# Kernel optimization log

Hardware: AMD Instinct MI355X
Metric: run time of the kernel (lower is better)

Reference implementation:

```python
import jax, jax.numpy as jnp
import numpy as np

B, S, HID = 2, 2048, 2048
H, D = 16, 128
BASE = 10000.0
NEG = -1e9


def _rope_tables(seq_len, dim, dtype):
    inv_freq = 1.0 / (BASE ** (jnp.arange(0, dim, 2, dtype=jnp.float32) / dim))
    pos = jnp.arange(seq_len, dtype=jnp.float32)
    freqs = jnp.einsum('s,d->sd', pos, inv_freq)          # [S, D/2]
    emb = jnp.concatenate([freqs, freqs], axis=-1)        # [S, D]
    return jnp.cos(emb).astype(dtype), jnp.sin(emb).astype(dtype)


def _rotate_half(x):
    x1, x2 = jnp.split(x, 2, axis=-1)
    return jnp.concatenate([-x2, x1], axis=-1)


def setup_inputs() -> dict:
    key = jax.random.key(0)
    k1, k2, k3 = jax.random.split(key, 3)
    x = jax.random.normal(k1, (B, S, HID), dtype=jnp.float32)
    w_qkv = jax.random.normal(k2, (HID, 3 * HID), dtype=jnp.float32) * (HID ** -0.5)
    w_out = jax.random.normal(k3, (HID, HID), dtype=jnp.float32) * (HID ** -0.5)
    return {"x": x, "w_qkv": w_qkv, "w_out": w_out}


def reference(x, w_qkv, w_out):
    b, s, _ = x.shape
    qkv = x @ w_qkv                                        # [B, S, 3*HID]
    qkv = qkv.reshape(b, s, 3, H, D).transpose(2, 0, 3, 1, 4)  # [3, B, H, S, D]
    q, k, v = qkv[0], qkv[1], qkv[2]
    cos, sin = _rope_tables(s, D, x.dtype)                 # [S, D]
    cos = cos[None, None]
    sin = sin[None, None]
    q = q * cos + _rotate_half(q) * sin
    k = k * cos + _rotate_half(k) * sin
    scale = 1.0 / np.sqrt(D)
    scores = jnp.einsum('bhqd,bhkd->bhqk', q, k) * scale   # [B, H, S, S]
    causal = jnp.triu(jnp.ones((s, s), dtype=bool), k=1)
    scores = jnp.where(causal[None, None], NEG, scores)
    attn = jax.nn.softmax(scores, axis=-1)
    out = jnp.einsum('bhqk,bhkd->bhqd', attn, v)           # [B, H, S, D]
    out = out.transpose(0, 2, 1, 3).reshape(b, s, H * D)
    return out @ w_out
```

## Files before the change

### kernel.cpp

```cpp
#include <hip/hip_runtime.h>
#include <hip/hip_bf16.h>

#define S_LEN 2048
#define HID_DIM 2048
#define NH 16
#define HD 128
#define N3 6144

typedef __bf16 bf16x8 __attribute__((ext_vector_type(8)));
typedef float f32x4 __attribute__((ext_vector_type(4)));
typedef float f32x16 __attribute__((ext_vector_type(16)));

#define MFMA16(a, b, c) __builtin_amdgcn_mfma_f32_16x16x32_bf16(a, b, c, 0, 0, 0)
#define MFMA32(a, b, c) __builtin_amdgcn_mfma_f32_32x32x16_bf16(a, b, c, 0, 0, 0)

__device__ __forceinline__ unsigned short f2bf(float f) {
  union { float f; unsigned u; } v; v.f = f;
  return (unsigned short)((v.u + 0x7fffu + ((v.u >> 16) & 1u)) >> 16);
}
__device__ __forceinline__ float bf2f(unsigned short h) {
  union { unsigned u; float f; } v; v.u = ((unsigned)h) << 16; return v.f;
}
__device__ __forceinline__ unsigned packbf2(float lo, float hi) {
  union { __hip_bfloat162 h2; unsigned u; } cv;
  cv.h2 = __float22bfloat162_rn(make_float2(lo, hi));
  return cv.u;
}
__device__ __forceinline__ void store_c(float* p, float v) { *p = v; }
__device__ __forceinline__ void store_c(unsigned short* p, float v) { *p = f2bf(v); }

__device__ __forceinline__ void async16(const void* g, void* l) {
  __builtin_amdgcn_global_load_lds((const __attribute__((address_space(1))) unsigned int*)g,
                                   (__attribute__((address_space(3))) unsigned int*)l,
                                   16, 0, 0);
}

template <int N> __device__ __forceinline__ void vmcnt();
template <> __device__ __forceinline__ void vmcnt<0>() { asm volatile("s_waitcnt vmcnt(0)" ::: "memory"); }
template <> __device__ __forceinline__ void vmcnt<5>() { asm volatile("s_waitcnt vmcnt(5)" ::: "memory"); }
template <> __device__ __forceinline__ void vmcnt<6>() { asm volatile("s_waitcnt vmcnt(6)" ::: "memory"); }

__global__ __launch_bounds__(256) void cast_bf16(const float4* __restrict__ src,
                                                 ushort4* __restrict__ dst) {
  int i = blockIdx.x * 256 + threadIdx.x;
  float4 v = src[i];
  ushort4 o;
  o.x = f2bf(v.x); o.y = f2bf(v.y); o.z = f2bf(v.z); o.w = f2bf(v.w);
  dst[i] = o;
}

__global__ __launch_bounds__(256) void transpose_cast(const float* __restrict__ src,
                                                      unsigned short* __restrict__ dst,
                                                      int R, int Ccols) {
  __shared__ float t[32][33];
  int ct = Ccols >> 5;
  int bx = blockIdx.x % ct, by = blockIdx.x / ct;
  int c0 = bx << 5, r0 = by << 5;
  int lx = threadIdx.x & 31, ly = threadIdx.x >> 5;
#pragma unroll
  for (int i = 0; i < 32; i += 8)
    t[ly + i][lx] = src[(long long)(r0 + ly + i) * Ccols + c0 + lx];
  __syncthreads();
#pragma unroll
  for (int i = 0; i < 32; i += 8)
    dst[(long long)(c0 + ly + i) * R + r0 + lx] = f2bf(t[lx][ly + i]);
}

__global__ __launch_bounds__(256) void rope_tables(float* __restrict__ cosT,
                                                   float* __restrict__ sinT) {
  int idx = blockIdx.x * 256 + threadIdx.x;
  int s = idx >> 6, i = idx & 63;
  float invf = powf(10000.0f, -(float)i * (1.0f / 64.0f));
  float a = (float)s * invf;
  cosT[idx] = cosf(a);
  sinT[idx] = sinf(a);
}

template <int BM, int BN, typename OutT>
__global__ __launch_bounds__(512) void gemm_pipe8(const unsigned short* __restrict__ A,
                                                  const unsigned short* __restrict__ Bt,
                                                  OutT* __restrict__ C,
                                                  int Mdim, int Ndim, int Kdim) {
  constexpr int WTM = BM / 2, WTN = BN / 4;
  constexpr int MREP = WTM / 16, NREP = WTN / 16;
  constexpr int AEL = BM * 64, BEL = BN * 64, BUFE = AEL + BEL;
  constexpr int AINST = BM / 64, BINST = BN / 64;
  constexpr int AHALF = BM / 128, BHALF = BN / 128;
  constexpr int VN = BN / 64 + BM / 128;
  __shared__ unsigned short smem[2 * BUFE];

  const int ntn = Ndim / BN;
  const int nwg = (Mdim / BM) * ntn;
  int bid = blockIdx.x;
  bid = (bid & 7) * (nwg >> 3) + (bid >> 3);
  const int tm = (bid / ntn) * BM;
  const int tn = (bid % ntn) * BN;

  const int tid = threadIdx.x;
  const int w = tid >> 6, l = tid & 63;
  const int g = l >> 4, cc = l & 15;
  const int wm = w >> 2, wn = w & 3;

  const int srow = tid >> 3;
  const int schunk = (tid & 7) ^ (srow & 7);
  const unsigned short* gA = A + (long long)(tm + srow) * Kdim + schunk * 8;
  const unsigned short* gB = Bt + (long long)(tn + srow) * Kdim + schunk * 8;

  const int ch0 = ((g) ^ (cc & 7)) << 3;
  const int ch1 = ((4 + g) ^ (cc & 7)) << 3;

  f32x4 acc[MREP][NREP] = {};
  bf16x8 a[MREP / 2][2], b[NREP][2];

  const int nk = Kdim >> 6;

#define STAGE_A(kt2, s) \
  async16(gA + (long long)(s) * 64 * Kdim + ((long long)(kt2) << 6), \
          smem + ((kt2) & 1) * BUFE + (s) * 4096 + w * 512)
#define STAGE_B(kt2, s) \
  async16(gB + (long long)(s) * 64 * Kdim + ((long long)(kt2) << 6), \
          smem + ((kt2) & 1) * BUFE + AEL + (s) * 4096 + w * 512)

#pragma unroll
  for (int s = 0; s < AINST; ++s) STAGE_A(0, s);
#pragma unroll
  for (int s = 0; s < BINST; ++s) STAGE_B(0, s);
#pragma unroll
  for (int s = 0; s < BINST; ++s) STAGE_B(1, s);
#pragma unroll
  for (int s = 0; s < AHALF; ++s) STAGE_A(1, s);
  vmcnt<VN>();
  __builtin_amdgcn_s_barrier();

  for (int kt = 0; kt < nk; ++kt) {
    const int buf = kt & 1;
    const unsigned short* Ab = smem + buf * BUFE + (wm * WTM) * 64;
    const unsigned short* Bb = smem + buf * BUFE + AEL + (wn * WTN) * 64;

#pragma unroll
    for (int i = 0; i < MREP / 2; ++i) {
      const int r = (i * 16 + cc) << 6;
      a[i][0] = *(const bf16x8*)(Ab + r + ch0);
      a[i][1] = *(const bf16x8*)(Ab + r + ch1);
    }
#pragma unroll
    for (int j = 0; j < NREP; ++j) {
      const int r = (j * 16 + cc) << 6;
      b[j][0] = *(const bf16x8*)(Bb + r + ch0);
      b[j][1] = *(const bf16x8*)(Bb + r + ch1);
    }
    if (kt + 1 < nk) {
#pragma unroll
      for (int s = AHALF; s < AINST; ++s) STAGE_A(kt + 1, s);
    }
    __builtin_amdgcn_s_barrier();
    __builtin_amdgcn_s_setprio(1);
#pragma unroll
    for (int i = 0; i < MREP / 2; ++i)
#pragma unroll
      for (int j = 0; j < NREP / 2; ++j) {
        acc[i][j] = MFMA16(a[i][0], b[j][0], acc[i][j]);
        acc[i][j] = MFMA16(a[i][1], b[j][1], acc[i][j]);
      }
    __builtin_amdgcn_s_setprio(0);
    __builtin_amdgcn_s_barrier();

    if (kt + 2 < nk) {
#pragma unroll
      for (int s = 0; s < BHALF; ++s) STAGE_B(kt + 2, s);
    }
    __builtin_amdgcn_s_barrier();
    __builtin_amdgcn_s_setprio(1);
#pragma unroll
    for (int i = 0; i < MREP / 2; ++i)
#pragma unroll
      for (int j = 0; j < NREP / 2; ++j) {
        f32x4& ac = acc[i][NREP / 2 + j];
        ac = MFMA16(a[i][0], b[NREP / 2 + j][0], ac);
        ac = MFMA16(a[i][1], b[NREP / 2 + j][1], ac);
      }
    __builtin_amdgcn_s_setprio(0);
    __builtin_amdgcn_s_barrier();

#pragma unroll
    for (int i = 0; i < MREP / 2; ++i) {
      const int r = ((WTM / 2) + i * 16 + cc) << 6;
      a[i][0] = *(const bf16x8*)(Ab + r + ch0);
      a[i][1] = *(const bf16x8*)(Ab + r + ch1);
    }
    if (kt + 2 < nk) {
#pragma unroll
      for (int s = BHALF; s < BINST; ++s) STAGE_B(kt + 2, s);
    }
    __builtin_amdgcn_s_barrier();
    __builtin_amdgcn_s_setprio(1);
#pragma unroll
    for (int i = 0; i < MREP / 2; ++i)
#pragma unroll
      for (int j = 0; j < NREP / 2; ++j) {
        f32x4& ac = acc[MREP / 2 + i][j];
        ac = MFMA16(a[i][0], b[j][0], ac);
        ac = MFMA16(a[i][1], b[j][1], ac);
      }
    __builtin_amdgcn_s_setprio(0);
    __builtin_amdgcn_s_barrier();

    if (kt + 2 < nk) {
#pragma unroll
      for (int s = 0; s < AHALF; ++s) STAGE_A(kt + 2, s);
    }
    __builtin_amdgcn_s_barrier();
    __builtin_amdgcn_s_setprio(1);
#pragma unroll
    for (int i = 0; i < MREP / 2; ++i)
#pragma unroll
      for (int j = 0; j < NREP / 2; ++j) {
        f32x4& ac = acc[MREP / 2 + i][NREP / 2 + j];
        ac = MFMA16(a[i][0], b[NREP / 2 + j][0], ac);
        ac = MFMA16(a[i][1], b[NREP / 2 + j][1], ac);
      }
    __builtin_amdgcn_s_setprio(0);
    if (kt + 2 < nk) vmcnt<VN>(); else vmcnt<0>();
    __builtin_amdgcn_s_barrier();
  }
#undef STAGE_A
#undef STAGE_B

  const int crow0 = tm + wm * WTM;
  const int ccol0 = tn + wn * WTN;
#pragma unroll
  for (int i = 0; i < MREP; ++i)
#pragma unroll
    for (int j = 0; j < NREP; ++j)
#pragma unroll
      for (int p = 0; p < 4; ++p) {
        int row = crow0 + i * 16 + (g << 2) + p;
        int col = ccol0 + j * 16 + cc;
        store_c(&C[(long long)row * Ndim + col], acc[i][j][p]);
      }
}

__global__ __launch_bounds__(256) void split_rope(const unsigned short* __restrict__ qkv,
                                                  const float* __restrict__ cosT,
                                                  const float* __restrict__ sinT,
                                                  unsigned short* __restrict__ Qb,
                                                  unsigned short* __restrict__ Kb,
                                                  unsigned short* __restrict__ Vt) {
  __shared__ unsigned short vtile[32][128];
  const int bid = blockIdx.x;
  const int st = bid & 63;
  const int h = (bid >> 6) & 15;
  const int b = bid >> 10;
  const int s0 = st << 5;
  const int t = threadIdx.x;
  const int d = t & 127;
  const int sl0 = t >> 7;
  const int dh = d & 63;
  const float sgn = (d < 64) ? -1.0f : 1.0f;
  const float qscale = 0.08838834764831845f;
#pragma unroll
  for (int it = 0; it < 16; ++it) {
    const int sl = sl0 + (it << 1);
    const int s = s0 + sl;
    const long long rb = ((long long)(b * S_LEN + s)) * N3 + h * HD;
    const float cv = cosT[(s << 6) + dh];
    const float sv = sinT[(s << 6) + dh];
    float qv = bf2f(qkv[rb + d]);
    float qo = bf2f(qkv[rb + (d ^ 64)]);
    float kv = bf2f(qkv[rb + HID_DIM + d]);
    float ko = bf2f(qkv[rb + HID_DIM + (d ^ 64)]);
    const long long ob = ((long long)((b * NH + h) * S_LEN + s)) * HD + d;
    Qb[ob] = f2bf((qv * cv + sgn * qo * sv) * qscale);
    Kb[ob] = f2bf(kv * cv + sgn * ko * sv);
    vtile[sl][d] = qkv[rb + 2 * HID_DIM + d];
  }
  __syncthreads();
  const int dr = t >> 1;
  const int sh = (t & 1) << 4;
  unsigned short tv[16];
#pragma unroll
  for (int j = 0; j < 16; ++j) tv[j] = vtile[sh + j][dr];
  uint4 u0, u1;
  u0.x = (unsigned)tv[0] | ((unsigned)tv[1] << 16);
  u0.y = (unsigned)tv[2] | ((unsigned)tv[3] << 16);
  u0.z = (unsigned)tv[4] | ((unsigned)tv[5] << 16);
  u0.w = (unsigned)tv[6] | ((unsigned)tv[7] << 16);
  u1.x = (unsigned)tv[8] | ((unsigned)tv[9] << 16);
  u1.y = (unsigned)tv[10] | ((unsigned)tv[11] << 16);
  u1.z = (unsigned)tv[12] | ((unsigned)tv[13] << 16);
  u1.w = (unsigned)tv[14] | ((unsigned)tv[15] << 16);
  const long long vb = ((long long)((b * NH + h) * HD + dr)) * S_LEN + s0 + sh;
  *(uint4*)(Vt + vb) = u0;
  *(uint4*)(Vt + vb + 8) = u1;
}

__global__ __launch_bounds__(256) void flash_attn(const unsigned short* __restrict__ Qg,
                                                  const unsigned short* __restrict__ Kg,
                                                  const unsigned short* __restrict__ Vt,
                                                  unsigned short* __restrict__ Ob) {
  __shared__ unsigned short smem[32768];
  const int id = blockIdx.x;
  const int bh = id & 31;
  const int qtr = (id >> 5) & 7;
  const int qt = (id >> 8) ? qtr : 15 - qtr;
  const int Q0 = qt << 7;
  const int b = bh >> 4, h = bh & 15;
  const long long base = (long long)bh * (S_LEN * HD);
  const int tid = threadIdx.x, w = tid >> 6, l = tid & 63;
  const int hi = l >> 5, q = l & 31;
  const int q0w = Q0 + (w << 5);
  const int g = l >> 4, c = l & 15;

  bf16x8 qf[8];
  {
    const unsigned short* qp = Qg + base + (long long)(q0w + q) * HD + (hi << 3);
#pragma unroll
    for (int s = 0; s < 8; ++s) qf[s] = *(const bf16x8*)(qp + (s << 4));
  }

  f32x16 oacc[4] = {};
  float m = -1e30f, lsum = 0.f;

  const int nt = (qt << 1) + 2;

  auto STAGE = [&](int kv0, int buf) {
    unsigned short* ks = smem + buf * 8192;
    unsigned short* vs = smem + 16384 + buf * 8192;
#pragma unroll
    for (int j = 0; j < 4; ++j) {
      int row = (w << 4) + (j << 2) + g;
      int chunk = c ^ (row & 7);
      async16(Kg + base + (long long)(kv0 + row) * HD + (chunk << 3),
              ks + (((w << 4) + (j << 2)) << 7));
    }
#pragma unroll
    for (int j = 0; j < 4; ++j) {
      int dr = (w << 5) + (j << 3) + (l >> 3);
      int chunk = (l & 7) ^ (dr & 7);
      async16(Vt + base + (long long)dr * S_LEN + kv0 + (chunk << 3),
              vs + (((w << 5) + (j << 3)) << 6));
    }
  };

  STAGE(0, 0);
  __syncthreads();

  int cur = 0;
  for (int t = 0; t < nt; ++t) {
    const int kv0 = t << 6;
    if (t + 1 < nt) STAGE((t + 1) << 6, cur ^ 1);

    if (kv0 < q0w + 32) {
      const unsigned short* ks = smem + cur * 8192;
      const unsigned short* vs = smem + 16384 + cur * 8192;

      f32x16 sa[2] = {};
#pragma unroll
      for (int h2 = 0; h2 < 2; ++h2) {
        const char* kb = (const char*)ks + (((h2 << 5) + q) << 8);
        const int r7 = q & 7;
#pragma unroll
        for (int s = 0; s < 8; ++s) {
          bf16x8 kf = *(const bf16x8*)(kb + ((((s << 1) + hi) ^ r7) << 4));
          sa[h2] = MFMA32(kf, qf[s], sa[h2]);
        }
      }

      if (kv0 + 63 > q0w) {
        const int qq = q0w + q;
#pragma unroll
        for (int h2 = 0; h2 < 2; ++h2)
#pragma unroll
          for (int j = 0; j < 16; ++j) {
            int kv = kv0 + (h2 << 5) + (j & 3) + ((j >> 2) << 3) + (hi << 2);
            if (kv > qq) sa[h2][j] = -1e30f;
          }
      }

      float tmax = -1e30f;
#pragma unroll
      for (int h2 = 0; h2 < 2; ++h2)
#pragma unroll
        for (int j = 0; j < 16; ++j) tmax = fmaxf(tmax, sa[h2][j]);
      tmax = fmaxf(tmax, __shfl_xor(tmax, 32));
      float mn = fmaxf(m, tmax);
      float fsc = __expf(m - mn);
      m = mn;
      float ps = 0.f;
#pragma unroll
      for (int h2 = 0; h2 < 2; ++h2)
#pragma unroll
        for (int j = 0; j < 16; ++j) {
          float pv = __expf(sa[h2][j] - mn);
          sa[h2][j] = pv;
          ps += pv;
        }
      ps += __shfl_xor(ps, 32);
      lsum = lsum * fsc + ps;
#pragma unroll
      for (int db = 0; db < 4; ++db)
#pragma unroll
        for (int j = 0; j < 16; ++j) oacc[db][j] *= fsc;

      unsigned up[2][8], wp[2][8];
#pragma unroll
      for (int h2 = 0; h2 < 2; ++h2)
#pragma unroll
        for (int k = 0; k < 8; ++k)
          up[h2][k] = packbf2(sa[h2][2 * k], sa[h2][2 * k + 1]);
#pragma unroll
      for (int h2 = 0; h2 < 2; ++h2)
#pragma unroll
        for (int k = 0; k < 8; ++k)
          wp[h2][k] = __shfl_xor((int)up[h2][k], 32);
      union Frag { unsigned u[4]; bf16x8 v; } pf[4];
#pragma unroll
      for (int s = 0; s < 4; ++s) {
        int h2 = s >> 1, q4 = (s & 1) << 2;
        pf[s].u[0] = hi ? wp[h2][q4 + 2] : up[h2][q4];
        pf[s].u[1] = hi ? wp[h2][q4 + 3] : up[h2][q4 + 1];
        pf[s].u[2] = hi ? up[h2][q4 + 2] : wp[h2][q4];
        pf[s].u[3] = hi ? up[h2][q4 + 3] : wp[h2][q4 + 1];
      }

#pragma unroll
      for (int db = 0; db < 4; ++db) {
        const char* vb = (const char*)vs + (((db << 5) + q) << 7);
        const int d7 = q & 7;
#pragma unroll
        for (int s = 0; s < 4; ++s) {
          bf16x8 vf = *(const bf16x8*)(vb + ((((s << 1) + hi) ^ d7) << 4));
          oacc[db] = MFMA32(vf, pf[s].v, oacc[db]);
        }
      }
    }

    __syncthreads();
    cur ^= 1;
  }

  const float rl = 1.0f / lsum;
#pragma unroll
  for (int db = 0; db < 4; ++db)
#pragma unroll
    for (int jg = 0; jg < 4; ++jg) {
      int d = (db << 5) + (jg << 3) + (hi << 2);
      unsigned v0 = packbf2(oacc[db][4 * jg] * rl, oacc[db][4 * jg + 1] * rl);
      unsigned v1 = packbf2(oacc[db][4 * jg + 2] * rl, oacc[db][4 * jg + 3] * rl);
      *(uint2*)(smem + (((w << 5) + q) << 7) + d) = make_uint2(v0, v1);
    }
  __syncthreads();
  {
    const int qr = tid >> 1;
    const int dh = (tid & 1) << 6;
    const uint4* src = (const uint4*)(smem + (qr << 7) + dh);
    uint4* dst = (uint4*)(Ob + (long long)((b << 11) + Q0 + qr) * HID_DIM + (h << 7) + dh);
#pragma unroll
    for (int cc2 = 0; cc2 < 8; ++cc2) dst[cc2] = src[cc2];
  }
}

extern "C" void kernel_launch(void* const* d_in, const int* in_sizes, int n_in,
                              void* d_out, int out_size, void* d_ws, size_t ws_size,
                              hipStream_t stream) {
  (void)in_sizes; (void)n_in; (void)out_size; (void)ws_size;
  const float* x = (const float*)d_in[0];
  const float* w_qkv = (const float*)d_in[1];
  const float* w_out = (const float*)d_in[2];
  float* out = (float*)d_out;
  char* ws = (char*)d_ws;

  unsigned short* xb    = (unsigned short*)(ws);
  unsigned short* wqkvT = (unsigned short*)(ws + 16777216);
  unsigned short* woutT = (unsigned short*)(ws + 41943040);
  unsigned short* qkv   = (unsigned short*)(ws + 50331648);
  unsigned short* Qb    = (unsigned short*)(ws + 100663296);
  unsigned short* Kb    = (unsigned short*)(ws + 117440512);
  unsigned short* Vt    = (unsigned short*)(ws + 134217728);
  float* cosT = (float*)(ws + 150994944);
  float* sinT = (float*)(ws + 151519232);
  unsigned short* Ob = qkv;

  cast_bf16<<<8192, 256, 0, stream>>>((const float4*)x, (ushort4*)xb);
  transpose_cast<<<12288, 256, 0, stream>>>(w_qkv, wqkvT, 2048, 6144);
  transpose_cast<<<4096, 256, 0, stream>>>(w_out, woutT, 2048, 2048);
  rope_tables<<<512, 256, 0, stream>>>(cosT, sinT);
  gemm_pipe8<256, 256, unsigned short><<<384, 512, 0, stream>>>(xb, wqkvT, qkv, 4096, 6144, 2048);
  split_rope<<<2048, 256, 0, stream>>>(qkv, cosT, sinT, Qb, Kb, Vt);
  flash_attn<<<512, 256, 0, stream>>>(Qb, Kb, Vt, Ob);
  gemm_pipe8<128, 256, float><<<256, 512, 0, stream>>>(Ob, woutT, out, 4096, 2048, 2048);
}
```

Before: 298.8 us.

## Add dedicated 256x192-tile QKV GEMM kernel with interleaved load/MFMA pipeline

```diff
diff --git a/kernel.cpp b/kernel.cpp
--- a/kernel.cpp
+++ b/kernel.cpp
@@ -38,7 +38,6 @@
 template <int N> __device__ __forceinline__ void vmcnt();
 template <> __device__ __forceinline__ void vmcnt<0>() { asm volatile("s_waitcnt vmcnt(0)" ::: "memory"); }
 template <> __device__ __forceinline__ void vmcnt<5>() { asm volatile("s_waitcnt vmcnt(5)" ::: "memory"); }
-template <> __device__ __forceinline__ void vmcnt<6>() { asm volatile("s_waitcnt vmcnt(6)" ::: "memory"); }
 
 __global__ __launch_bounds__(256) void cast_bf16(const float4* __restrict__ src,
                                                  ushort4* __restrict__ dst) {
@@ -74,6 +73,146 @@
   float a = (float)s * invf;
   cosT[idx] = cosf(a);
   sinT[idx] = sinf(a);
+}
+
+__global__ __launch_bounds__(512) void gemm_qkv(const unsigned short* __restrict__ A,
+                                                const unsigned short* __restrict__ Bt,
+                                                unsigned short* __restrict__ C,
+                                                int Mdim, int Ndim, int Kdim) {
+  constexpr int AEL = 256 * 64;
+  constexpr int BEL = 192 * 64;
+  constexpr int BUFE = AEL + BEL;
+  __shared__ unsigned short smem[2 * BUFE];
+
+  const int ntn = Ndim / 192;
+  const int nwg = (Mdim >> 8) * ntn;
+  int bid = blockIdx.x;
+  bid = (bid & 7) * (nwg >> 3) + (bid >> 3);
+  const int tm = (bid / ntn) << 8;
+  const int tn = (bid % ntn) * 192;
+
+  const int tid = threadIdx.x;
+  const int w = tid >> 6, l = tid & 63;
+  const int g = l >> 4, cc = l & 15;
+  const int wm = w >> 2, wn = w & 3;
+
+  const int srow = tid >> 3;
+  const int schunk = (tid & 7) ^ (srow & 7);
+  const unsigned short* gA = A + (long long)(tm + srow) * Kdim + schunk * 8;
+  const unsigned short* gB = Bt + (long long)(tn + srow) * Kdim + schunk * 8;
+
+  const int ch0 = ((g) ^ (cc & 7)) << 3;
+  const int ch1 = ((4 + g) ^ (cc & 7)) << 3;
+
+  f32x4 acc[8][3] = {};
+  bf16x8 a[4][2], b[3][2];
+  const int nk = Kdim >> 6;
+
+#define ST_A(kt2, BUF, s) \
+  async16(gA + (long long)(s) * 64 * Kdim + ((long long)(kt2) << 6), \
+          smem + (BUF) * BUFE + (s) * 4096 + w * 512)
+#define ST_B(kt2, BUF, s) \
+  async16(gB + (long long)(s) * 64 * Kdim + ((long long)(kt2) << 6), \
+          smem + (BUF) * BUFE + AEL + (s) * 4096 + w * 512)
+
+#pragma unroll
+  for (int s = 0; s < 4; ++s) ST_A(0, 0, s);
+#pragma unroll
+  for (int s = 0; s < 3; ++s) ST_B(0, 0, s);
+  ST_A(1, 1, 0); ST_A(1, 1, 2);
+  ST_B(1, 1, 0); ST_B(1, 1, 1); ST_B(1, 1, 2);
+  vmcnt<5>();
+  __builtin_amdgcn_s_barrier();
+
+#define KSTEP(kt, BUF, OBUF)                                                      \
+  {                                                                               \
+    const unsigned short* Ab = smem + (BUF) * BUFE + wm * (128 * 64);             \
+    const unsigned short* Bb = smem + (BUF) * BUFE + AEL + wn * (48 * 64);        \
+      \
+    _Pragma("unroll") for (int i = 0; i < 4; ++i) {                               \
+      const int r = (i * 16 + cc) << 6;                                           \
+      a[i][0] = *(const bf16x8*)(Ab + r + ch0);                                   \
+      a[i][1] = *(const bf16x8*)(Ab + r + ch1);                                   \
+    }                                                                             \
+    _Pragma("unroll") for (int j = 0; j < 2; ++j) {                               \
+      const int r = (j * 16 + cc) << 6;                                           \
+      b[j][0] = *(const bf16x8*)(Bb + r + ch0);                                   \
+      b[j][1] = *(const bf16x8*)(Bb + r + ch1);                                   \
+    }                                                                             \
+    if ((kt) + 1 < nk) { ST_A((kt) + 1, OBUF, 1); ST_A((kt) + 1, OBUF, 3); }      \
+    __builtin_amdgcn_s_barrier();                                                 \
+    __builtin_amdgcn_s_setprio(1);                                                \
+    _Pragma("unroll") for (int i = 0; i < 4; ++i)                                 \
+      _Pragma("unroll") for (int j = 0; j < 2; ++j) {                             \
+        acc[i][j] = MFMA16(a[i][0], b[j][0], acc[i][j]);                          \
+        acc[i][j] = MFMA16(a[i][1], b[j][1], acc[i][j]);                          \
+      }                                                                           \
+    __builtin_amdgcn_s_setprio(0);                                                \
+    __builtin_amdgcn_s_barrier();                                                 \
+                   \
+    {                                                                             \
+      const int r = (2 * 16 + cc) << 6;                                           \
+      b[2][0] = *(const bf16x8*)(Bb + r + ch0);                                   \
+      b[2][1] = *(const bf16x8*)(Bb + r + ch1);                                   \
+    }                                                                             \
+    if ((kt) + 2 < nk) { ST_A((kt) + 2, BUF, 0); ST_A((kt) + 2, BUF, 2); }        \
+    __builtin_amdgcn_s_barrier();                                                 \
+    __builtin_amdgcn_s_setprio(1);                                                \
+    _Pragma("unroll") for (int i = 0; i < 4; ++i) {                               \
+      acc[i][2] = MFMA16(a[i][0], b[2][0], acc[i][2]);                            \
+      acc[i][2] = MFMA16(a[i][1], b[2][1], acc[i][2]);                            \
+    }                                                                             \
+    __builtin_amdgcn_s_setprio(0);                                                \
+    __builtin_amdgcn_s_barrier();                                                 \
+            \
+    _Pragma("unroll") for (int i = 0; i < 4; ++i) {                               \
+      const int r = ((64 + i * 16 + cc) << 6);                                    \
+      a[i][0] = *(const bf16x8*)(Ab + r + ch0);                                   \
+      a[i][1] = *(const bf16x8*)(Ab + r + ch1);                                   \
+    }                                                                             \
+    if ((kt) + 2 < nk) { ST_B((kt) + 2, BUF, 0); ST_B((kt) + 2, BUF, 1); }        \
+    __builtin_amdgcn_s_barrier();                                                 \
+    __builtin_amdgcn_s_setprio(1);                                                \
+    _Pragma("unroll") for (int i = 0; i < 4; ++i)                                 \
+      _Pragma("unroll") for (int j = 0; j < 2; ++j) {                             \
+        acc[4 + i][j] = MFMA16(a[i][0], b[j][0], acc[4 + i][j]);                  \
+        acc[4 + i][j] = MFMA16(a[i][1], b[j][1], acc[4 + i][j]);                  \
+      }                                                                           \
+    __builtin_amdgcn_s_setprio(0);                                                \
+    __builtin_amdgcn_s_barrier();                                                 \
+               \
+    if ((kt) + 2 < nk) { ST_B((kt) + 2, BUF, 2); }                                \
+    __builtin_amdgcn_s_barrier();                                                 \
+    __builtin_amdgcn_s_setprio(1);                                                \
+    _Pragma("unroll") for (int i = 0; i < 4; ++i) {                               \
+      acc[4 + i][2] = MFMA16(a[i][0], b[2][0], acc[4 + i][2]);                    \
+      acc[4 + i][2] = MFMA16(a[i][1], b[2][1], acc[4 + i][2]);                    \
+    }                                                                             \
+    __builtin_amdgcn_s_setprio(0);                                                \
+    if ((kt) + 2 < nk) vmcnt<5>(); else vmcnt<0>();                               \
+    __builtin_amdgcn_s_barrier();                                                 \
+  }
+
+  for (int kt = 0; kt < nk; kt += 2) {
+    KSTEP(kt, 0, 1);
+    KSTEP(kt + 1, 1, 0);
+  }
+#undef KSTEP
+#undef ST_A
+#undef ST_B
+
+  const int crow0 = tm + wm * 128;
+  const int ccol0 = tn + wn * 48;
+#pragma unroll
+  for (int mi = 0; mi < 8; ++mi)
+#pragma unroll
+    for (int j = 0; j < 3; ++j)
+#pragma unroll
+      for (int p = 0; p < 4; ++p) {
+        int row = crow0 + ((mi >> 2) << 6) + ((mi & 3) << 4) + (g << 2) + p;
+        int col = ccol0 + j * 16 + cc;
+        store_c(&C[(long long)row * Ndim + col], acc[mi][j][p]);
+      }
 }
 
 template <int BM, int BN, typename OutT>
@@ -485,7 +624,7 @@
   transpose_cast<<<12288, 256, 0, stream>>>(w_qkv, wqkvT, 2048, 6144);
   transpose_cast<<<4096, 256, 0, stream>>>(w_out, woutT, 2048, 2048);
   rope_tables<<<512, 256, 0, stream>>>(cosT, sinT);
-  gemm_pipe8<256, 256, unsigned short><<<384, 512, 0, stream>>>(xb, wqkvT, qkv, 4096, 6144, 2048);
+  gemm_qkv<<<512, 512, 0, stream>>>(xb, wqkvT, qkv, 4096, 6144, 2048);
   split_rope<<<2048, 256, 0, stream>>>(qkv, cosT, sinT, Qb, Kb, Vt);
   flash_attn<<<512, 256, 0, stream>>>(Qb, Kb, Vt, Ob);
   gemm_pipe8<128, 256, float><<<256, 512, 0, stream>>>(Ob, woutT, out, 4096, 2048, 2048);
```

Result: faster. 286.9 us (-4.0%).
